# Kernel tuning notes

Hardware: AMD Instinct MI355X
Metric: run time of the kernel (lower is better)

Reference implementation:

```python
import jax, jax.numpy as jnp
import numpy as np

N, S, D, H, E, ETYPES = 1024, 64, 256, 4, 4096, 4
HD = D // H
EPS = 1e-5


def setup_inputs() -> dict:
    key = jax.random.key(0)
    ks = jax.random.split(key, 8)
    node_features = jax.random.normal(ks[0], (N, S, D), dtype=jnp.float32)
    lengths = jax.random.randint(ks[1], (N,), 1, S + 1)
    node_masks = (jnp.arange(S)[None, :] < lengths[:, None]).astype(jnp.float32)
    # unique edges (torch builds an adjacency matrix, so duplicates collapse)
    rng = np.random.default_rng(0)
    cand = rng.integers(0, N, size=(4 * E, 2))
    uniq = np.unique(cand, axis=0)
    assert uniq.shape[0] >= E
    perm = rng.permutation(uniq.shape[0])[:E]
    edge_index = jnp.asarray(uniq[perm].T, dtype=jnp.int64)  # [2, E]
    edge_type = jnp.asarray(rng.integers(1, ETYPES + 1, size=(E,)), dtype=jnp.int64)
    scale = 0.02
    wq = jax.random.normal(ks[2], (D, D), jnp.float32) * scale
    wk = jax.random.normal(ks[3], (D, D), jnp.float32) * scale
    wv = jax.random.normal(ks[4], (D, D), jnp.float32) * scale
    wo = jax.random.normal(ks[5], (D, D), jnp.float32) * scale
    return dict(
        node_features=node_features, node_masks=node_masks,
        ln_w=jnp.ones((D,), jnp.float32), ln_b=jnp.zeros((D,), jnp.float32),
        wq=wq, bq=jnp.zeros((D,), jnp.float32),
        wk=wk, bk=jnp.zeros((D,), jnp.float32),
        wv=wv, bv=jnp.zeros((D,), jnp.float32),
        wo=wo, bo=jnp.zeros((D,), jnp.float32),
        edge_type_weights=jnp.ones((ETYPES,), jnp.float32),
        edge_index=edge_index, edge_type=edge_type,
    )


def reference(node_features, node_masks, ln_w, ln_b, wq, bq, wk, bk, wv, bv,
              wo, bo, edge_type_weights, edge_index, edge_type):
    n, s, d = node_features.shape
    # LayerNorm (biased variance, eps=1e-5, as torch)
    mu = jnp.mean(node_features, axis=-1, keepdims=True)
    var = jnp.mean((node_features - mu) ** 2, axis=-1, keepdims=True)
    xn = (node_features - mu) * jax.lax.rsqrt(var + EPS) * ln_w + ln_b
    q = (xn @ wq + bq).reshape(n, s, H, HD)
    k = (xn @ wk + bk).reshape(n, s, H, HD)
    v = (xn @ wv + bv).reshape(n, s, H, HD)
    src, dst = edge_index[0], edge_index[1]
    # per-edge scalar bias: softplus(edge_type_weights[type-1]).clamp(1e-6, 1e6)
    ew = jnp.clip(jax.nn.softplus(edge_type_weights[edge_type - 1]), 1e-6, 1e6)  # [E]
    qe, ke, ve = q[src], k[dst], v[dst]              # [E,S,H,HD]
    km = node_masks[dst]                              # [E,S] key-side mask
    qm = node_masks[src]                              # [E,S] query-side mask
    scores = jnp.einsum('eqhd,ekhd->ehqk', qe, ke) / jnp.sqrt(jnp.float32(HD))
    scores = scores + ew[:, None, None, None]
    neg = jnp.float32(-1e30)
    scores = jnp.where(km[:, None, None, :] > 0, scores, neg)
    # per-edge softmax over the key node's valid tokens; zero rows where no valid key
    attn = jax.nn.softmax(scores, axis=-1) * km[:, None, None, :]
    ctx = jnp.einsum('ehqk,ekhd->eqhd', attn, ve) * qm[:, :, None, None]  # [E,S,H,HD]
    out = jax.ops.segment_sum(ctx, src, num_segments=n)   # sum over incident edges
    out = out.reshape(n, s, d)
    out = out @ wo + bo                                   # output projection (dropout=eval noop)
    out = out + node_features                             # residual
    return out * node_masks[..., None]
```

## Files before the change

### kernel.cpp

```cpp
#include <hip/hip_runtime.h>

#define DDIM 256
#define NEDGE 4096
#define SLEN 64
#define NNODE 1024
#define ROWS 65536

typedef short s16x8 __attribute__((ext_vector_type(8)));
typedef float f32x4 __attribute__((ext_vector_type(4)));

static __device__ __forceinline__ unsigned short f2bf(float f){
  union { float f; unsigned u; } v; v.f = f;
  unsigned r = v.u + 0x7FFFu + ((v.u >> 16) & 1u);
  return (unsigned short)(r >> 16);
}

static __device__ __forceinline__ void gl2lds16(const unsigned short* g, unsigned short* l){
  __builtin_amdgcn_global_load_lds((const __attribute__((address_space(1))) unsigned int*)g,
                                   (__attribute__((address_space(3))) unsigned int*)l, 16, 0, 0);
}

__global__ __launch_bounds__(256) void setup_kernel(const float* nf, const float* lnw, const float* lnb,
                                                    const float* wq, const float* wk, const float* wv, const float* wo,
                                                    const float* bq, const float* bk, const float* bv,
                                                    const float* masks,
                                                    unsigned short* xn, unsigned short* Wqkv, unsigned short* Wo_t,
                                                    float* qkvb, int* lenp){
  int bid = blockIdx.x, tid = threadIdx.x;
  if (bid < 16384){
    int lane = tid & 63;
    int row = bid*4 + (tid >> 6);
    const float4 x4 = ((const float4*)(nf + (size_t)row*DDIM))[lane];
    float s  = x4.x + x4.y + x4.z + x4.w;
    float sq = x4.x*x4.x + x4.y*x4.y + x4.z*x4.z + x4.w*x4.w;
    for (int off=1; off<64; off<<=1){ s += __shfl_xor(s, off); sq += __shfl_xor(sq, off); }
    float mu  = s  * (1.0f/DDIM);
    float var = sq * (1.0f/DDIM) - mu*mu;
    float rs  = rsqrtf(var + 1e-5f);
    float4 w4 = ((const float4*)lnw)[lane];
    float4 b4 = ((const float4*)lnb)[lane];
    ushort4 o;
    o.x = f2bf((x4.x - mu)*rs*w4.x + b4.x);
    o.y = f2bf((x4.y - mu)*rs*w4.y + b4.y);
    o.z = f2bf((x4.z - mu)*rs*w4.z + b4.z);
    o.w = f2bf((x4.w - mu)*rs*w4.w + b4.w);
    ((ushort4*)(xn + (size_t)row*DDIM))[lane] = o;
  } else if (bid < 17412){
    int idx = (bid - 16384)*256 + tid;
    if (idx < 196608){
      int mat = idx >> 16;
      int rem = idx & 65535;
      int n = rem >> 8, k = rem & 255;
      const float* W = (mat==0)?wq:(mat==1)?wk:wv;
      Wqkv[(size_t)(mat*256 + n)*256 + k] = f2bf(W[k*256 + n]);
    } else if (idx < 262144){
      int rem = idx - 196608;
      int n = rem >> 8, k = rem & 255;
      Wo_t[(size_t)n*256 + k] = f2bf(wo[k*256 + n]);
    } else if (idx < 262912){
      int i = idx - 262144;
      qkvb[i] = (i < 256) ? bq[i] : (i < 512) ? bk[i-256] : bv[i-512];
    }
  } else {
    int lane = tid & 63;
    int node = (bid - 17412)*4 + (tid >> 6);
    unsigned long long b = __ballot(masks[node*SLEN + lane] > 0.f);
    if (lane == 0) lenp[node] = __popcll(b);
  }
}

__global__ void csr_kernel(const int* eidx, int* startp, int* order, int* degp, int* elist){
  __shared__ int deg[NNODE];
  __shared__ int buf[NNODE];
  __shared__ int hist[65];
  __shared__ int cur[NNODE];
  int t = threadIdx.x;
  deg[t] = 0;
  if (t < 65) hist[t] = 0;
  __syncthreads();
  #pragma unroll
  for (int i=0;i<4;i++) atomicAdd(&deg[eidx[i*1024 + t]], 1);
  __syncthreads();
  int d = deg[t];
  buf[t] = d;
  __syncthreads();
  for (int off=1; off<NNODE; off<<=1){
    int v = (t >= off) ? buf[t-off] : 0;
    __syncthreads();
    buf[t] += v;
    __syncthreads();
  }
  int st = buf[t] - d;
  startp[t] = st; degp[t] = d; cur[t] = st;
  int dc = d > 64 ? 64 : d;
  atomicAdd(&hist[dc], 1);
  __syncthreads();
  if (t == 0){
    int acc = 0;
    for (int i=64;i>=0;i--){ int h = hist[i]; hist[i] = acc; acc += h; }
  }
  __syncthreads();
  int pos = atomicAdd(&hist[dc], 1);
  order[pos] = t;
  __syncthreads();
  #pragma unroll
  for (int i=0;i<4;i++){
    int e = i*1024 + t;
    int s = eidx[e];
    int p = atomicAdd(&cur[s], 1);
    elist[p] = eidx[NEDGE + e];
  }
}

__global__ __launch_bounds__(256) void qkv_kernel(const unsigned short* xn, const unsigned short* Wqkv,
                                                  const float* qkvb, const int* lenp,
                                                  unsigned short* qb, unsigned short* kb_, unsigned short* vt){
  __shared__ __align__(16) unsigned short As[4096];
  __shared__ __align__(16) unsigned short Bs[8192];
  int tid = threadIdx.x;
  int lane = tid & 63, wid = tid >> 6, m = lane & 15, quad = lane >> 4;
  int row0 = blockIdx.x * 64;
  int node = row0 >> 6;
  int qtm = (lenp[node] + 15) >> 4;
  int vrows = qtm << 4;
  int col0 = blockIdx.y * 128;
  int rw = (wid & 1) * 32, cw = (wid >> 1) * 64;
  int t0 = rw >> 4;
  f32x4 acc[8];
  #pragma unroll
  for (int i=0;i<8;i++) acc[i] = (f32x4){0.f,0.f,0.f,0.f};
  for (int kc = 0; kc < 4; kc++){
    __syncthreads();
    #pragma unroll
    for (int i=0;i<2;i++){
      if (i*32 + wid*8 < vrows){
        int cid = i*256 + tid, row = cid >> 3, c8 = cid & 7;
        gl2lds16(xn + (size_t)(row0 + row)*DDIM + kc*64 + ((c8 ^ (row&7))<<3), As + cid*8);
      }
    }
    #pragma unroll
    for (int i=0;i<4;i++){
      int cid = i*256 + tid, row = cid >> 3, c8 = cid & 7;
      gl2lds16(Wqkv + (size_t)(col0 + row)*DDIM + kc*64 + ((c8 ^ (row&7))<<3), Bs + cid*8);
    }
    __syncthreads();
    #pragma unroll
    for (int ks=0; ks<2; ks++){
      int sw = ((ks*4 + quad) ^ (m&7)) << 3;
      s16x8 af[2], bf[4];
      #pragma unroll
      for (int mt=0;mt<2;mt++) if (t0 + mt < qtm) af[mt] = *(const s16x8*)(As + (rw + mt*16 + m)*64 + sw);
      #pragma unroll
      for (int nt=0;nt<4;nt++) bf[nt] = *(const s16x8*)(Bs + (cw + nt*16 + m)*64 + sw);
      #pragma unroll
      for (int mt=0;mt<2;mt++) if (t0 + mt < qtm)
        #pragma unroll
        for (int nt=0;nt<4;nt++)
          acc[mt*4+nt] = __builtin_amdgcn_mfma_f32_16x16x32_bf16(af[mt], bf[nt], acc[mt*4+nt], 0,0,0);
    }
  }
  #pragma unroll
  for (int nt=0;nt<4;nt++){
    int cg = col0 + cw + nt*16 + m;
    int mat = cg >> 8, col = cg & 255;
    float bb = qkvb[cg];
    if (mat < 2){
      unsigned short* ob = (mat==0)?qb:kb_;
      #pragma unroll
      for (int mt=0;mt<2;mt++) if (t0 + mt < qtm)
        #pragma unroll
        for (int r=0;r<4;r++){
          int row = row0 + rw + mt*16 + quad*4 + r;
          ob[(size_t)row*DDIM + col] = f2bf(acc[mt*4+nt][r] + bb);
        }
    } else {
      #pragma unroll
      for (int mt=0;mt<2;mt++) if (t0 + mt < qtm){
        int tok0 = rw + mt*16 + quad*4;
        ushort4 p;
        p.x = f2bf(acc[mt*4+nt][0] + bb);
        p.y = f2bf(acc[mt*4+nt][1] + bb);
        p.z = f2bf(acc[mt*4+nt][2] + bb);
        p.w = f2bf(acc[mt*4+nt][3] + bb);
        *(ushort4*)(vt + ((size_t)node*256 + col)*64 + tok0) = p;
      }
    }
  }
}

__global__ __launch_bounds__(256) void attn_kernel(const unsigned short* qb, const unsigned short* kbuf,
                                                   const unsigned short* vtb, const int* lenp,
                                                   const int* startp, const int* degp, const int* elist,
                                                   const int* order, unsigned short* ctxb){
  __shared__ __align__(16) unsigned short Kt[2][4096];
  __shared__ __align__(16) unsigned short Vt[2][4096];
  __shared__ unsigned short P[4096];
  int tid = threadIdx.x;
  int lane = tid & 63, wid = tid >> 6, m = lane & 15, quad = lane >> 4;
  int src = order[blockIdx.x], h = blockIdx.y;
  int ls = lenp[src];
  int qtm = (ls + 15) >> 4;
  int s0 = startp[src], dg = degp[src];
  bool active = wid < qtm;
  unsigned short* Pw = P + wid*1024;

  s16x8 qf0 = {0,0,0,0,0,0,0,0}, qf1 = {0,0,0,0,0,0,0,0};
  if (active){
    const unsigned short* qbase = qb + (size_t)(src*SLEN + wid*16 + m)*DDIM + h*64 + quad*8;
    qf0 = *(const s16x8*)(qbase);
    qf1 = *(const s16x8*)(qbase + 32);
  }
  f32x4 o[4];
  #pragma unroll
  for (int i=0;i<4;i++) o[i] = (f32x4){0.f,0.f,0.f,0.f};

  int dst0 = 0, dst1 = 0, ld0 = 0;
  if (dg > 0){
    dst0 = elist[s0];
    ld0 = lenp[dst0];
    int kch = ((ld0 + 15) >> 4) * 128;
    #pragma unroll
    for (int i=0;i<2;i++){
      int cid = i*256 + tid;
      if (i*256 + wid*64 < kch){
        int row = cid >> 3, c8 = cid & 7;
        gl2lds16(kbuf + (size_t)(dst0*SLEN + row)*DDIM + h*64 + ((c8 ^ (row&7))<<3), Kt[0] + cid*8);
      }
    }
    const unsigned short* vhead = vtb + ((size_t)dst0*256 + h*64)*64;
    #pragma unroll
    for (int i=0;i<2;i++){
      int cid = i*256 + tid, row = cid >> 3, c8 = cid & 7;
      gl2lds16(vhead + row*64 + ((c8 ^ (row&7))<<3), Vt[0] + cid*8);
    }
  }
  if (dg > 1) dst1 = elist[s0 + 1];
  __syncthreads();

  for (int ei=0; ei<dg; ei++){
    int cur = ei & 1, nxt = cur ^ 1;
    int dst2 = (ei+2 < dg) ? elist[s0 + ei + 2] : 0;
    int ld1 = 0;
    if (ei+1 < dg){
      ld1 = lenp[dst1];
      int kch = ((ld1 + 15) >> 4) * 128;
      #pragma unroll
      for (int i=0;i<2;i++){
        int cid = i*256 + tid;
        if (i*256 + wid*64 < kch){
          int row = cid >> 3, c8 = cid & 7;
          gl2lds16(kbuf + (size_t)(dst1*SLEN + row)*DDIM + h*64 + ((c8 ^ (row&7))<<3), Kt[nxt] + cid*8);
        }
      }
      const unsigned short* vhead = vtb + ((size_t)dst1*256 + h*64)*64;
      #pragma unroll
      for (int i=0;i<2;i++){
        int cid = i*256 + tid, row = cid >> 3, c8 = cid & 7;
        gl2lds16(vhead + row*64 + ((c8 ^ (row&7))<<3), Vt[nxt] + cid*8);
      }
    }
    int ktm = (ld0 + 15) >> 4;
    int ks2 = (ktm + 1) >> 1;
    if (active){
      f32x4 acc[4];
      #pragma unroll
      for (int i=0;i<4;i++) acc[i] = (f32x4){0.f,0.f,0.f,0.f};
      #pragma unroll
      for (int kt=0; kt<4; kt++) if (kt < ktm){
        int key = kt*16 + m;
        s16x8 b0 = *(const s16x8*)(Kt[cur] + key*64 + ((quad ^ (m&7))<<3));
        acc[kt] = __builtin_amdgcn_mfma_f32_16x16x32_bf16(qf0, b0, acc[kt], 0,0,0);
        s16x8 b1 = *(const s16x8*)(Kt[cur] + key*64 + (((4 + quad) ^ (m&7))<<3));
        acc[kt] = __builtin_amdgcn_mfma_f32_16x16x32_bf16(qf1, b1, acc[kt], 0,0,0);
      }
      #pragma unroll
      for (int r=0; r<4; r++){
        float x[4];
        #pragma unroll
        for (int kt=0; kt<4; kt++)
          x[kt] = (kt < ktm && kt*16 + m < ld0) ? __expf(acc[kt][r]*0.125f) : 0.f;
        float s = x[0] + x[1] + x[2] + x[3];
        for (int off=1; off<16; off<<=1) s += __shfl_xor(s, off);
        float inv = 1.0f / s;
        int q = quad*4 + r;
        #pragma unroll
        for (int kt=0; kt<4; kt++) if (kt < 2*ks2){
          int key = kt*16 + m;
          Pw[q*64 + (((key>>3)^(q&7))<<3) + (key&7)] = f2bf(x[kt]*inv);
        }
      }
      #pragma unroll
      for (int ks=0; ks<2; ks++) if (ks < ks2){
        s16x8 pa = *(const s16x8*)(Pw + m*64 + ((((ks*4+quad))^(m&7))<<3));
        #pragma unroll
        for (int dt=0; dt<4; dt++){
          int d = dt*16 + m;
          s16x8 vf = *(const s16x8*)(Vt[cur] + d*64 + (((ks*4+quad)^(d&7))<<3));
          o[dt] = __builtin_amdgcn_mfma_f32_16x16x32_bf16(pa, vf, o[dt], 0,0,0);
        }
      }
    }
    dst0 = dst1; ld0 = ld1; dst1 = dst2;
    __syncthreads();
  }
  if (active){
    #pragma unroll
    for (int dt=0; dt<4; dt++){
      int col = h*64 + dt*16 + m;
      #pragma unroll
      for (int r=0; r<4; r++){
        int row = src*SLEN + wid*16 + quad*4 + r;
        ctxb[(size_t)row*DDIM + col] = f2bf(o[dt][r]);
      }
    }
  }
}

__global__ __launch_bounds__(256) void out_kernel(const unsigned short* ctxb, const unsigned short* Wo_t,
                                                  const float* bo, const float* nf, const float* masks,
                                                  const int* lenp, float* out){
  __shared__ __align__(16) unsigned short As[4096];
  __shared__ __align__(16) unsigned short Bs[8192];
  int tid = threadIdx.x;
  int lane = tid & 63, wid = tid >> 6, m = lane & 15, quad = lane >> 4;
  int row0 = blockIdx.x * 64;
  int node = row0 >> 6;
  int qtm = (lenp[node] + 15) >> 4;
  int vrows = qtm << 4;
  int col0 = blockIdx.y * 128;
  int rw = (wid & 1) * 32, cw = (wid >> 1) * 64;
  int t0 = rw >> 4;
  f32x4 acc[8];
  #pragma unroll
  for (int i=0;i<8;i++) acc[i] = (f32x4){0.f,0.f,0.f,0.f};
  for (int kc = 0; kc < 4; kc++){
    __syncthreads();
    #pragma unroll
    for (int i=0;i<2;i++){
      if (i*32 + wid*8 < vrows){
        int cid = i*256 + tid, row = cid >> 3, c8 = cid & 7;
        gl2lds16(ctxb + (size_t)(row0 + row)*DDIM + kc*64 + ((c8 ^ (row&7))<<3), As + cid*8);
      }
    }
    #pragma unroll
    for (int i=0;i<4;i++){
      int cid = i*256 + tid, row = cid >> 3, c8 = cid & 7;
      gl2lds16(Wo_t + (size_t)(col0 + row)*DDIM + kc*64 + ((c8 ^ (row&7))<<3), Bs + cid*8);
    }
    __syncthreads();
    #pragma unroll
    for (int ks=0; ks<2; ks++){
      int sw = ((ks*4 + quad) ^ (m&7)) << 3;
      s16x8 af[2], bf[4];
      #pragma unroll
      for (int mt=0;mt<2;mt++) if (t0 + mt < qtm) af[mt] = *(const s16x8*)(As + (rw + mt*16 + m)*64 + sw);
      #pragma unroll
      for (int nt=0;nt<4;nt++) bf[nt] = *(const s16x8*)(Bs + (cw + nt*16 + m)*64 + sw);
      #pragma unroll
      for (int mt=0;mt<2;mt++) if (t0 + mt < qtm)
        #pragma unroll
        for (int nt=0;nt<4;nt++)
          acc[mt*4+nt] = __builtin_amdgcn_mfma_f32_16x16x32_bf16(af[mt], bf[nt], acc[mt*4+nt], 0,0,0);
    }
  }
  #pragma unroll
  for (int nt=0;nt<4;nt++){
    int col = col0 + cw + nt*16 + m;
    float bb = bo[col];
    #pragma unroll
    for (int mt=0;mt<2;mt++){
      if (t0 + mt < qtm){
        #pragma unroll
        for (int r=0;r<4;r++){
          int row = row0 + rw + mt*16 + quad*4 + r;
          float v = acc[mt*4+nt][r] + bb + nf[(size_t)row*DDIM + col];
          out[(size_t)row*DDIM + col] = v * masks[row];
        }
      } else {
        #pragma unroll
        for (int r=0;r<4;r++){
          int row = row0 + rw + mt*16 + quad*4 + r;
          out[(size_t)row*DDIM + col] = 0.f;
        }
      }
    }
  }
}

extern "C" void kernel_launch(void* const* d_in, const int* in_sizes, int n_in,
                              void* d_out, int out_size, void* d_ws, size_t ws_size,
                              hipStream_t stream){
  const float* nf    = (const float*)d_in[0];
  const float* masks = (const float*)d_in[1];
  const float* lnw   = (const float*)d_in[2];
  const float* lnb   = (const float*)d_in[3];
  const float* wq    = (const float*)d_in[4];
  const float* bq    = (const float*)d_in[5];
  const float* wk    = (const float*)d_in[6];
  const float* bk    = (const float*)d_in[7];
  const float* wv    = (const float*)d_in[8];
  const float* bv    = (const float*)d_in[9];
  const float* wo    = (const float*)d_in[10];
  const float* bo    = (const float*)d_in[11];
  const int*   eidx  = (const int*)d_in[13];
  float* out = (float*)d_out;

  char* ws = (char*)d_ws;
  const size_t B = (size_t)ROWS * DDIM * 2;
  unsigned short* xn   = (unsigned short*)(ws);
  unsigned short* qb   = (unsigned short*)(ws + B);
  unsigned short* kb   = (unsigned short*)(ws + 2*B);
  unsigned short* vt   = (unsigned short*)(ws + 3*B);
  unsigned short* ctxb = (unsigned short*)(ws + 4*B);
  char* wp = ws + 5*B;
  unsigned short* Wqkv = (unsigned short*)(wp);
  unsigned short* Wo_t = (unsigned short*)(wp + 393216);
  float* qkvb         = (float*)(wp + 524288);
  char* ip = wp + 528384;
  int* startp = (int*)(ip);
  int* lenp   = (int*)(ip + 4096);
  int* order  = (int*)(ip + 8192);
  int* degp   = (int*)(ip + 12288);
  int* elist  = (int*)(ip + 16384);

  setup_kernel<<<17668, 256, 0, stream>>>(nf, lnw, lnb, wq, wk, wv, wo, bq, bk, bv,
                                          masks, xn, Wqkv, Wo_t, qkvb, lenp);
  csr_kernel<<<1, 1024, 0, stream>>>(eidx, startp, order, degp, elist);
  qkv_kernel<<<dim3(ROWS/64, 6), 256, 0, stream>>>(xn, Wqkv, qkvb, lenp, qb, kb, vt);
  attn_kernel<<<dim3(NNODE, 4), 256, 0, stream>>>(qb, kb, vt, lenp, startp, degp, elist, order, ctxb);
  out_kernel<<<dim3(ROWS/64, 2), 256, 0, stream>>>(ctxb, Wo_t, bo, nf, masks, lenp, out);
}
```

Before: 345.7 us.

## Restructure QKV and output GEMMs to direct-load per-node tiles; skip padded LN rows

The QKV and output projection kernels no longer stage tiles in LDS. Each block now covers one node's full 64 rows, and each wave loads its bf16 fragments straight from global memory for 64 columns. Q is stored transposed (feature-major) like V, so the attention kernel gathers Q fragments with strided scalar loads. LayerNorm also returns early for rows past the node's 16-padded valid length, and the output kernel zero-fills padded rows with vector stores. This removes LDS traffic, barriers and redundant A-tile loads, at the cost of uncoalesced global fragment loads and a strided scalar Q gather.

```diff
diff --git a/kernel.cpp b/kernel.cpp
--- a/kernel.cpp
+++ b/kernel.cpp
@@ -30,6 +30,11 @@
   if (bid < 16384){
     int lane = tid & 63;
     int row = bid*4 + (tid >> 6);
+    int node = row >> 6;
+    unsigned long long bm = __ballot(masks[node*SLEN + lane] > 0.f);
+    int len = __popcll(bm);
+    int vrows = ((len + 15) >> 4) << 4;
+    if ((row & 63) >= vrows) return;
     const float4 x4 = ((const float4*)(nf + (size_t)row*DDIM))[lane];
     float s  = x4.x + x4.y + x4.z + x4.w;
     float sq = x4.x*x4.x + x4.y*x4.y + x4.z*x4.z + x4.w*x4.w;
@@ -114,81 +119,65 @@
 
 __global__ __launch_bounds__(256) void qkv_kernel(const unsigned short* xn, const unsigned short* Wqkv,
                                                   const float* qkvb, const int* lenp,
-                                                  unsigned short* qb, unsigned short* kb_, unsigned short* vt){
-  __shared__ __align__(16) unsigned short As[4096];
-  __shared__ __align__(16) unsigned short Bs[8192];
+                                                  unsigned short* qt, unsigned short* kb_, unsigned short* vt){
   int tid = threadIdx.x;
   int lane = tid & 63, wid = tid >> 6, m = lane & 15, quad = lane >> 4;
-  int row0 = blockIdx.x * 64;
-  int node = row0 >> 6;
+  int node = blockIdx.x;
+  int row0 = node * 64;
   int qtm = (lenp[node] + 15) >> 4;
-  int vrows = qtm << 4;
-  int col0 = blockIdx.y * 128;
-  int rw = (wid & 1) * 32, cw = (wid >> 1) * 64;
-  int t0 = rw >> 4;
-  f32x4 acc[8];
-  #pragma unroll
-  for (int i=0;i<8;i++) acc[i] = (f32x4){0.f,0.f,0.f,0.f};
-  for (int kc = 0; kc < 4; kc++){
-    __syncthreads();
-    #pragma unroll
-    for (int i=0;i<2;i++){
-      if (i*32 + wid*8 < vrows){
-        int cid = i*256 + tid, row = cid >> 3, c8 = cid & 7;
-        gl2lds16(xn + (size_t)(row0 + row)*DDIM + kc*64 + ((c8 ^ (row&7))<<3), As + cid*8);
-      }
-    }
-    #pragma unroll
-    for (int i=0;i<4;i++){
-      int cid = i*256 + tid, row = cid >> 3, c8 = cid & 7;
-      gl2lds16(Wqkv + (size_t)(col0 + row)*DDIM + kc*64 + ((c8 ^ (row&7))<<3), Bs + cid*8);
-    }
-    __syncthreads();
-    #pragma unroll
-    for (int ks=0; ks<2; ks++){
-      int sw = ((ks*4 + quad) ^ (m&7)) << 3;
-      s16x8 af[2], bf[4];
-      #pragma unroll
-      for (int mt=0;mt<2;mt++) if (t0 + mt < qtm) af[mt] = *(const s16x8*)(As + (rw + mt*16 + m)*64 + sw);
-      #pragma unroll
-      for (int nt=0;nt<4;nt++) bf[nt] = *(const s16x8*)(Bs + (cw + nt*16 + m)*64 + sw);
-      #pragma unroll
-      for (int mt=0;mt<2;mt++) if (t0 + mt < qtm)
-        #pragma unroll
-        for (int nt=0;nt<4;nt++)
-          acc[mt*4+nt] = __builtin_amdgcn_mfma_f32_16x16x32_bf16(af[mt], bf[nt], acc[mt*4+nt], 0,0,0);
-    }
-  }
-  #pragma unroll
-  for (int nt=0;nt<4;nt++){
-    int cg = col0 + cw + nt*16 + m;
-    int mat = cg >> 8, col = cg & 255;
-    float bb = qkvb[cg];
-    if (mat < 2){
-      unsigned short* ob = (mat==0)?qb:kb_;
-      #pragma unroll
-      for (int mt=0;mt<2;mt++) if (t0 + mt < qtm)
+  int by = blockIdx.y;
+  int cb = wid * 64;
+  f32x4 acc[16];
+  #pragma unroll
+  for (int i=0;i<16;i++) acc[i] = (f32x4){0.f,0.f,0.f,0.f};
+  const unsigned short* ab = xn   + (size_t)(row0 + m)*DDIM + quad*8;
+  const unsigned short* bb = Wqkv + ((size_t)by*256 + cb + m)*DDIM + quad*8;
+  #pragma unroll
+  for (int ks=0; ks<8; ks++){
+    s16x8 bf[4];
+    #pragma unroll
+    for (int nt=0;nt<4;nt++) bf[nt] = *(const s16x8*)(bb + nt*16*DDIM + ks*32);
+    #pragma unroll
+    for (int mt=0;mt<4;mt++) if (mt < qtm){
+      s16x8 af = *(const s16x8*)(ab + mt*16*DDIM + ks*32);
+      #pragma unroll
+      for (int nt=0;nt<4;nt++)
+        acc[mt*4+nt] = __builtin_amdgcn_mfma_f32_16x16x32_bf16(af, bf[nt], acc[mt*4+nt], 0,0,0);
+    }
+  }
+  if (by != 1){
+    unsigned short* dst = (by==0) ? qt : vt;
+    #pragma unroll
+    for (int nt=0;nt<4;nt++){
+      int col = cb + nt*16 + m;
+      float bbv = qkvb[by*256 + col];
+      #pragma unroll
+      for (int mt=0;mt<4;mt++) if (mt < qtm){
+        ushort4 p;
+        p.x = f2bf(acc[mt*4+nt][0] + bbv);
+        p.y = f2bf(acc[mt*4+nt][1] + bbv);
+        p.z = f2bf(acc[mt*4+nt][2] + bbv);
+        p.w = f2bf(acc[mt*4+nt][3] + bbv);
+        *(ushort4*)(dst + ((size_t)node*256 + col)*64 + mt*16 + quad*4) = p;
+      }
+    }
+  } else {
+    #pragma unroll
+    for (int nt=0;nt<4;nt++){
+      int col = cb + nt*16 + m;
+      float bbv = qkvb[256 + col];
+      #pragma unroll
+      for (int mt=0;mt<4;mt++) if (mt < qtm)
         #pragma unroll
         for (int r=0;r<4;r++){
-          int row = row0 + rw + mt*16 + quad*4 + r;
-          ob[(size_t)row*DDIM + col] = f2bf(acc[mt*4+nt][r] + bb);
+          int row = row0 + mt*16 + quad*4 + r;
+          kb_[(size_t)row*DDIM + col] = f2bf(acc[mt*4+nt][r] + bbv);
         }
-    } else {
-      #pragma unroll
-      for (int mt=0;mt<2;mt++) if (t0 + mt < qtm){
-        int tok0 = rw + mt*16 + quad*4;
-        ushort4 p;
-        p.x = f2bf(acc[mt*4+nt][0] + bb);
-        p.y = f2bf(acc[mt*4+nt][1] + bb);
-        p.z = f2bf(acc[mt*4+nt][2] + bb);
-        p.w = f2bf(acc[mt*4+nt][3] + bb);
-        *(ushort4*)(vt + ((size_t)node*256 + col)*64 + tok0) = p;
-      }
-    }
-  }
-}
-
-__global__ __launch_bounds__(256) void attn_kernel(const unsigned short* qb, const unsigned short* kbuf,
+    }
+  }
+}
+
+__global__ __launch_bounds__(256) void attn_kernel(const unsigned short* qt, const unsigned short* kbuf,
                                                    const unsigned short* vtb, const int* lenp,
                                                    const int* startp, const int* degp, const int* elist,
                                                    const int* order, unsigned short* ctxb){
@@ -206,9 +195,13 @@
 
   s16x8 qf0 = {0,0,0,0,0,0,0,0}, qf1 = {0,0,0,0,0,0,0,0};
   if (active){
-    const unsigned short* qbase = qb + (size_t)(src*SLEN + wid*16 + m)*DDIM + h*64 + quad*8;
-    qf0 = *(const s16x8*)(qbase);
-    qf1 = *(const s16x8*)(qbase + 32);
+    const unsigned short* qtb = qt + ((size_t)src*256 + h*64)*64;
+    int tok = wid*16 + m;
+    #pragma unroll
+    for (int j=0;j<8;j++){
+      qf0[j] = (short)qtb[(quad*8 + j)*64 + tok];
+      qf1[j] = (short)qtb[(32 + quad*8 + j)*64 + tok];
+    }
   }
   f32x4 o[4];
   #pragma unroll
@@ -319,72 +312,46 @@
 __global__ __launch_bounds__(256) void out_kernel(const unsigned short* ctxb, const unsigned short* Wo_t,
                                                   const float* bo, const float* nf, const float* masks,
                                                   const int* lenp, float* out){
-  __shared__ __align__(16) unsigned short As[4096];
-  __shared__ __align__(16) unsigned short Bs[8192];
   int tid = threadIdx.x;
   int lane = tid & 63, wid = tid >> 6, m = lane & 15, quad = lane >> 4;
-  int row0 = blockIdx.x * 64;
-  int node = row0 >> 6;
+  int node = blockIdx.x;
+  int row0 = node * 64;
   int qtm = (lenp[node] + 15) >> 4;
   int vrows = qtm << 4;
-  int col0 = blockIdx.y * 128;
-  int rw = (wid & 1) * 32, cw = (wid >> 1) * 64;
-  int t0 = rw >> 4;
-  f32x4 acc[8];
-  #pragma unroll
-  for (int i=0;i<8;i++) acc[i] = (f32x4){0.f,0.f,0.f,0.f};
-  for (int kc = 0; kc < 4; kc++){
-    __syncthreads();
-    #pragma unroll
-    for (int i=0;i<2;i++){
-      if (i*32 + wid*8 < vrows){
-        int cid = i*256 + tid, row = cid >> 3, c8 = cid & 7;
-        gl2lds16(ctxb + (size_t)(row0 + row)*DDIM + kc*64 + ((c8 ^ (row&7))<<3), As + cid*8);
-      }
-    }
-    #pragma unroll
-    for (int i=0;i<4;i++){
-      int cid = i*256 + tid, row = cid >> 3, c8 = cid & 7;
-      gl2lds16(Wo_t + (size_t)(col0 + row)*DDIM + kc*64 + ((c8 ^ (row&7))<<3), Bs + cid*8);
-    }
-    __syncthreads();
-    #pragma unroll
-    for (int ks=0; ks<2; ks++){
-      int sw = ((ks*4 + quad) ^ (m&7)) << 3;
-      s16x8 af[2], bf[4];
-      #pragma unroll
-      for (int mt=0;mt<2;mt++) if (t0 + mt < qtm) af[mt] = *(const s16x8*)(As + (rw + mt*16 + m)*64 + sw);
-      #pragma unroll
-      for (int nt=0;nt<4;nt++) bf[nt] = *(const s16x8*)(Bs + (cw + nt*16 + m)*64 + sw);
-      #pragma unroll
-      for (int mt=0;mt<2;mt++) if (t0 + mt < qtm)
-        #pragma unroll
-        for (int nt=0;nt<4;nt++)
-          acc[mt*4+nt] = __builtin_amdgcn_mfma_f32_16x16x32_bf16(af[mt], bf[nt], acc[mt*4+nt], 0,0,0);
+  int cb = wid * 64;
+  f32x4 acc[16];
+  #pragma unroll
+  for (int i=0;i<16;i++) acc[i] = (f32x4){0.f,0.f,0.f,0.f};
+  const unsigned short* ab = ctxb + (size_t)(row0 + m)*DDIM + quad*8;
+  const unsigned short* bb = Wo_t + (size_t)(cb + m)*DDIM + quad*8;
+  #pragma unroll
+  for (int ks=0; ks<8; ks++){
+    s16x8 bf[4];
+    #pragma unroll
+    for (int nt=0;nt<4;nt++) bf[nt] = *(const s16x8*)(bb + nt*16*DDIM + ks*32);
+    #pragma unroll
+    for (int mt=0;mt<4;mt++) if (mt < qtm){
+      s16x8 af = *(const s16x8*)(ab + mt*16*DDIM + ks*32);
+      #pragma unroll
+      for (int nt=0;nt<4;nt++)
+        acc[mt*4+nt] = __builtin_amdgcn_mfma_f32_16x16x32_bf16(af, bf[nt], acc[mt*4+nt], 0,0,0);
     }
   }
   #pragma unroll
   for (int nt=0;nt<4;nt++){
-    int col = col0 + cw + nt*16 + m;
-    float bb = bo[col];
-    #pragma unroll
-    for (int mt=0;mt<2;mt++){
-      if (t0 + mt < qtm){
-        #pragma unroll
-        for (int r=0;r<4;r++){
-          int row = row0 + rw + mt*16 + quad*4 + r;
-          float v = acc[mt*4+nt][r] + bb + nf[(size_t)row*DDIM + col];
-          out[(size_t)row*DDIM + col] = v * masks[row];
-        }
-      } else {
-        #pragma unroll
-        for (int r=0;r<4;r++){
-          int row = row0 + rw + mt*16 + quad*4 + r;
-          out[(size_t)row*DDIM + col] = 0.f;
-        }
-      }
-    }
-  }
+    int col = cb + nt*16 + m;
+    float bbv = bo[col];
+    #pragma unroll
+    for (int mt=0;mt<4;mt++) if (mt < qtm)
+      #pragma unroll
+      for (int r=0;r<4;r++){
+        int row = row0 + mt*16 + quad*4 + r;
+        float v = acc[mt*4+nt][r] + bbv + nf[(size_t)row*DDIM + col];
+        out[(size_t)row*DDIM + col] = v * masks[row];
+      }
+  }
+  for (int r = vrows + wid; r < 64; r += 4)
+    ((float4*)(out + (size_t)(row0 + r)*DDIM))[lane] = (float4){0.f,0.f,0.f,0.f};
 }
 
 extern "C" void kernel_launch(void* const* d_in, const int* in_sizes, int n_in,
@@ -408,7 +375,7 @@
   char* ws = (char*)d_ws;
   const size_t B = (size_t)ROWS * DDIM * 2;
   unsigned short* xn   = (unsigned short*)(ws);
-  unsigned short* qb   = (unsigned short*)(ws + B);
+  unsigned short* qt   = (unsigned short*)(ws + B);
   unsigned short* kb   = (unsigned short*)(ws + 2*B);
   unsigned short* vt   = (unsigned short*)(ws + 3*B);
   unsigned short* ctxb = (unsigned short*)(ws + 4*B);
@@ -426,7 +393,7 @@
   setup_kernel<<<17668, 256, 0, stream>>>(nf, lnw, lnb, wq, wk, wv, wo, bq, bk, bv,
                                           masks, xn, Wqkv, Wo_t, qkvb, lenp);
   csr_kernel<<<1, 1024, 0, stream>>>(eidx, startp, order, degp, elist);
-  qkv_kernel<<<dim3(ROWS/64, 6), 256, 0, stream>>>(xn, Wqkv, qkvb, lenp, qb, kb, vt);
-  attn_kernel<<<dim3(NNODE, 4), 256, 0, stream>>>(qb, kb, vt, lenp, startp, degp, elist, order, ctxb);
-  out_kernel<<<dim3(ROWS/64, 2), 256, 0, stream>>>(ctxb, Wo_t, bo, nf, masks, lenp, out);
-}
+  qkv_kernel<<<dim3(NNODE, 3), 256, 0, stream>>>(xn, Wqkv, qkvb, lenp, qt, kb, vt);
+  attn_kernel<<<dim3(NNODE, 4), 256, 0, stream>>>(qt, kb, vt, lenp, startp, degp, elist, order, ctxb);
+  out_kernel<<<NNODE, 256, 0, stream>>>(ctxb, Wo_t, bo, nf, masks, lenp, out);
+}
```

Result: slower. 384.4 us (+11.2%).

## Merge CSR build into setup, skip padded LayerNorm rows, one block per node in attention

Applied to the files above, without the earlier changes.

The CSR build moves into an extra block of the setup kernel, removing one launch and its single-block serial tail. The LayerNorm path now skips rows beyond each node's padded valid length, since those rows are never read. Attention now runs one block per source node, with each wave handling one head across all query tiles. Each neighbour's full K/V tile is loaded once for all four heads instead of once per head, but the double-buffered prefetch is dropped and register pressure rises with 16 accumulators per wave.

```diff
diff --git a/kernel.cpp b/kernel.cpp
--- a/kernel.cpp
+++ b/kernel.cpp
@@ -23,13 +23,23 @@
 __global__ __launch_bounds__(256) void setup_kernel(const float* nf, const float* lnw, const float* lnb,
                                                     const float* wq, const float* wk, const float* wv, const float* wo,
                                                     const float* bq, const float* bk, const float* bv,
-                                                    const float* masks,
+                                                    const float* masks, const int* eidx,
                                                     unsigned short* xn, unsigned short* Wqkv, unsigned short* Wo_t,
-                                                    float* qkvb, int* lenp){
+                                                    float* qkvb, int* lenp,
+                                                    int* startp, int* order, int* degp, int* elist){
+  __shared__ int sdeg[NNODE];
+  __shared__ int sbuf[256];
+  __shared__ int scur[NNODE];
+  __shared__ int shist[65];
   int bid = blockIdx.x, tid = threadIdx.x;
   if (bid < 16384){
     int lane = tid & 63;
     int row = bid*4 + (tid >> 6);
+    int node = row >> 6;
+    unsigned long long bm = __ballot(masks[node*SLEN + lane] > 0.f);
+    int len = __popcll(bm);
+    int vrows = ((len + 15) >> 4) << 4;
+    if ((row & 63) >= vrows) return;
     const float4 x4 = ((const float4*)(nf + (size_t)row*DDIM))[lane];
     float s  = x4.x + x4.y + x4.z + x4.w;
     float sq = x4.x*x4.x + x4.y*x4.y + x4.z*x4.z + x4.w*x4.w;
@@ -61,54 +71,63 @@
       int i = idx - 262144;
       qkvb[i] = (i < 256) ? bq[i] : (i < 512) ? bk[i-256] : bv[i-512];
     }
-  } else {
+  } else if (bid < 17668){
     int lane = tid & 63;
     int node = (bid - 17412)*4 + (tid >> 6);
     unsigned long long b = __ballot(masks[node*SLEN + lane] > 0.f);
     if (lane == 0) lenp[node] = __popcll(b);
-  }
-}
-
-__global__ void csr_kernel(const int* eidx, int* startp, int* order, int* degp, int* elist){
-  __shared__ int deg[NNODE];
-  __shared__ int buf[NNODE];
-  __shared__ int hist[65];
-  __shared__ int cur[NNODE];
-  int t = threadIdx.x;
-  deg[t] = 0;
-  if (t < 65) hist[t] = 0;
-  __syncthreads();
-  #pragma unroll
-  for (int i=0;i<4;i++) atomicAdd(&deg[eidx[i*1024 + t]], 1);
-  __syncthreads();
-  int d = deg[t];
-  buf[t] = d;
-  __syncthreads();
-  for (int off=1; off<NNODE; off<<=1){
-    int v = (t >= off) ? buf[t-off] : 0;
-    __syncthreads();
-    buf[t] += v;
-    __syncthreads();
-  }
-  int st = buf[t] - d;
-  startp[t] = st; degp[t] = d; cur[t] = st;
-  int dc = d > 64 ? 64 : d;
-  atomicAdd(&hist[dc], 1);
-  __syncthreads();
-  if (t == 0){
-    int acc = 0;
-    for (int i=64;i>=0;i--){ int h = hist[i]; hist[i] = acc; acc += h; }
-  }
-  __syncthreads();
-  int pos = atomicAdd(&hist[dc], 1);
-  order[pos] = t;
-  __syncthreads();
-  #pragma unroll
-  for (int i=0;i<4;i++){
-    int e = i*1024 + t;
-    int s = eidx[e];
-    int p = atomicAdd(&cur[s], 1);
-    elist[p] = eidx[NEDGE + e];
+  } else {
+    int t = tid;
+    #pragma unroll
+    for (int i=0;i<4;i++) sdeg[i*256 + t] = 0;
+    if (t < 65) shist[t] = 0;
+    __syncthreads();
+    #pragma unroll
+    for (int i=0;i<16;i++) atomicAdd(&sdeg[eidx[i*256 + t]], 1);
+    __syncthreads();
+    int d[4];
+    #pragma unroll
+    for (int j=0;j<4;j++) d[j] = sdeg[t*4 + j];
+    int s = d[0] + d[1] + d[2] + d[3];
+    sbuf[t] = s;
+    __syncthreads();
+    for (int off=1; off<256; off<<=1){
+      int v = (t >= off) ? sbuf[t-off] : 0;
+      __syncthreads();
+      sbuf[t] += v;
+      __syncthreads();
+    }
+    int base = sbuf[t] - s;
+    int acc = base;
+    #pragma unroll
+    for (int j=0;j<4;j++){
+      int node = t*4 + j;
+      startp[node] = acc; degp[node] = d[j]; scur[node] = acc;
+      acc += d[j];
+      int dc = d[j] > 64 ? 64 : d[j];
+      atomicAdd(&shist[dc], 1);
+    }
+    __syncthreads();
+    if (t == 0){
+      int a = 0;
+      for (int i=64;i>=0;i--){ int h = shist[i]; shist[i] = a; a += h; }
+    }
+    __syncthreads();
+    #pragma unroll
+    for (int j=0;j<4;j++){
+      int node = t*4 + j;
+      int dc = d[j] > 64 ? 64 : d[j];
+      int pos = atomicAdd(&shist[dc], 1);
+      order[pos] = node;
+    }
+    __syncthreads();
+    #pragma unroll
+    for (int i=0;i<16;i++){
+      int e = i*256 + t;
+      int sn = eidx[e];
+      int p = atomicAdd(&scur[sn], 1);
+      elist[p] = eidx[NEDGE + e];
+    }
   }
 }
 
@@ -192,93 +211,73 @@
                                                    const unsigned short* vtb, const int* lenp,
                                                    const int* startp, const int* degp, const int* elist,
                                                    const int* order, unsigned short* ctxb){
-  __shared__ __align__(16) unsigned short Kt[2][4096];
-  __shared__ __align__(16) unsigned short Vt[2][4096];
+  __shared__ __align__(16) unsigned short Kf[16384];
+  __shared__ __align__(16) unsigned short Vf[16384];
   __shared__ unsigned short P[4096];
   int tid = threadIdx.x;
-  int lane = tid & 63, wid = tid >> 6, m = lane & 15, quad = lane >> 4;
-  int src = order[blockIdx.x], h = blockIdx.y;
+  int lane = tid & 63, h = tid >> 6, m = lane & 15, quad = lane >> 4;
+  int src = order[blockIdx.x];
   int ls = lenp[src];
   int qtm = (ls + 15) >> 4;
   int s0 = startp[src], dg = degp[src];
-  bool active = wid < qtm;
-  unsigned short* Pw = P + wid*1024;
-
-  s16x8 qf0 = {0,0,0,0,0,0,0,0}, qf1 = {0,0,0,0,0,0,0,0};
-  if (active){
-    const unsigned short* qbase = qb + (size_t)(src*SLEN + wid*16 + m)*DDIM + h*64 + quad*8;
-    qf0 = *(const s16x8*)(qbase);
-    qf1 = *(const s16x8*)(qbase + 32);
-  }
-  f32x4 o[4];
-  #pragma unroll
-  for (int i=0;i<4;i++) o[i] = (f32x4){0.f,0.f,0.f,0.f};
-
-  int dst0 = 0, dst1 = 0, ld0 = 0;
-  if (dg > 0){
-    dst0 = elist[s0];
-    ld0 = lenp[dst0];
-    int kch = ((ld0 + 15) >> 4) * 128;
-    #pragma unroll
-    for (int i=0;i<2;i++){
+  unsigned short* Pw = P + h*1024;
+
+  s16x8 qf[4][2];
+  #pragma unroll
+  for (int qt_=0; qt_<4; qt_++) if (qt_ < qtm){
+    const unsigned short* qbase = qb + (size_t)(src*SLEN + qt_*16 + m)*DDIM + h*64 + quad*8;
+    qf[qt_][0] = *(const s16x8*)(qbase);
+    qf[qt_][1] = *(const s16x8*)(qbase + 32);
+  }
+  f32x4 o[16];
+  #pragma unroll
+  for (int i=0;i<16;i++) o[i] = (f32x4){0.f,0.f,0.f,0.f};
+
+  int dst = 0, ld = 0;
+  if (dg > 0){ dst = elist[s0]; ld = lenp[dst]; }
+
+  for (int ei=0; ei<dg; ei++){
+    int dstn = (ei+1 < dg) ? elist[s0 + ei + 1] : 0;
+    int ktm = (ld + 15) >> 4;
+    int ks2 = (ktm + 1) >> 1;
+    int krows = ktm << 4;
+    __syncthreads();
+    #pragma unroll
+    for (int i=0;i<8;i++){
       int cid = i*256 + tid;
-      if (i*256 + wid*64 < kch){
-        int row = cid >> 3, c8 = cid & 7;
-        gl2lds16(kbuf + (size_t)(dst0*SLEN + row)*DDIM + h*64 + ((c8 ^ (row&7))<<3), Kt[0] + cid*8);
-      }
-    }
-    const unsigned short* vhead = vtb + ((size_t)dst0*256 + h*64)*64;
-    #pragma unroll
-    for (int i=0;i<2;i++){
-      int cid = i*256 + tid, row = cid >> 3, c8 = cid & 7;
-      gl2lds16(vhead + row*64 + ((c8 ^ (row&7))<<3), Vt[0] + cid*8);
-    }
-  }
-  if (dg > 1) dst1 = elist[s0 + 1];
-  __syncthreads();
-
-  for (int ei=0; ei<dg; ei++){
-    int cur = ei & 1, nxt = cur ^ 1;
-    int dst2 = (ei+2 < dg) ? elist[s0 + ei + 2] : 0;
-    int ld1 = 0;
-    if (ei+1 < dg){
-      ld1 = lenp[dst1];
-      int kch = ((ld1 + 15) >> 4) * 128;
-      #pragma unroll
-      for (int i=0;i<2;i++){
-        int cid = i*256 + tid;
-        if (i*256 + wid*64 < kch){
-          int row = cid >> 3, c8 = cid & 7;
-          gl2lds16(kbuf + (size_t)(dst1*SLEN + row)*DDIM + h*64 + ((c8 ^ (row&7))<<3), Kt[nxt] + cid*8);
-        }
-      }
-      const unsigned short* vhead = vtb + ((size_t)dst1*256 + h*64)*64;
-      #pragma unroll
-      for (int i=0;i<2;i++){
-        int cid = i*256 + tid, row = cid >> 3, c8 = cid & 7;
-        gl2lds16(vhead + row*64 + ((c8 ^ (row&7))<<3), Vt[nxt] + cid*8);
-      }
-    }
-    int ktm = (ld0 + 15) >> 4;
-    int ks2 = (ktm + 1) >> 1;
-    if (active){
+      int tok = cid >> 5;
+      if (tok < krows){
+        int within = cid & 31, seg = within >> 3, c8 = within & 7;
+        gl2lds16(kbuf + (size_t)(dst*SLEN + tok)*DDIM + seg*64 + ((c8 ^ (tok&7))<<3), Kf + cid*8);
+      }
+    }
+    #pragma unroll
+    for (int i=0;i<8;i++){
+      int cid = i*256 + tid;
+      int col = cid >> 3, t8 = cid & 7;
+      gl2lds16(vtb + ((size_t)dst*256 + col)*64 + ((t8 ^ (col&7))<<3), Vf + cid*8);
+    }
+    int ldn = (ei+1 < dg) ? lenp[dstn] : 0;
+    __syncthreads();
+    #pragma unroll
+    for (int qt_=0; qt_<4; qt_++) if (qt_ < qtm){
       f32x4 acc[4];
       #pragma unroll
       for (int i=0;i<4;i++) acc[i] = (f32x4){0.f,0.f,0.f,0.f};
       #pragma unroll
       for (int kt=0; kt<4; kt++) if (kt < ktm){
         int key = kt*16 + m;
-        s16x8 b0 = *(const s16x8*)(Kt[cur] + key*64 + ((quad ^ (m&7))<<3));
-        acc[kt] = __builtin_amdgcn_mfma_f32_16x16x32_bf16(qf0, b0, acc[kt], 0,0,0);
-        s16x8 b1 = *(const s16x8*)(Kt[cur] + key*64 + (((4 + quad) ^ (m&7))<<3));
-        acc[kt] = __builtin_amdgcn_mfma_f32_16x16x32_bf16(qf1, b1, acc[kt], 0,0,0);
+        s16x8 b0 = *(const s16x8*)(Kf + key*DDIM + h*64 + ((quad ^ (key&7))<<3));
+        acc[kt] = __builtin_amdgcn_mfma_f32_16x16x32_bf16(qf[qt_][0], b0, acc[kt], 0,0,0);
+        s16x8 b1 = *(const s16x8*)(Kf + key*DDIM + h*64 + (((4 + quad) ^ (key&7))<<3));
+        acc[kt] = __builtin_amdgcn_mfma_f32_16x16x32_bf16(qf[qt_][1], b1, acc[kt], 0,0,0);
       }
       #pragma unroll
       for (int r=0; r<4; r++){
         float x[4];
         #pragma unroll
         for (int kt=0; kt<4; kt++)
-          x[kt] = (kt < ktm && kt*16 + m < ld0) ? __expf(acc[kt][r]*0.125f) : 0.f;
+          x[kt] = (kt < ktm && kt*16 + m < ld) ? __expf(acc[kt][r]*0.125f) : 0.f;
         float s = x[0] + x[1] + x[2] + x[3];
         for (int off=1; off<16; off<<=1) s += __shfl_xor(s, off);
         float inv = 1.0f / s;
@@ -286,7 +285,7 @@
         #pragma unroll
         for (int kt=0; kt<4; kt++) if (kt < 2*ks2){
           int key = kt*16 + m;
-          Pw[q*64 + (((key>>3)^(q&7))<<3) + (key&7)] = f2bf(x[kt]*inv);
+          Pw[q*64 + (((key>>3)^(q&7))<<3) + (key&7)] = f2bf((kt < ktm) ? x[kt]*inv : 0.f);
         }
       }
       #pragma unroll
@@ -294,23 +293,23 @@
         s16x8 pa = *(const s16x8*)(Pw + m*64 + ((((ks*4+quad))^(m&7))<<3));
         #pragma unroll
         for (int dt=0; dt<4; dt++){
-          int d = dt*16 + m;
-          s16x8 vf = *(const s16x8*)(Vt[cur] + d*64 + (((ks*4+quad)^(d&7))<<3));
-          o[dt] = __builtin_amdgcn_mfma_f32_16x16x32_bf16(pa, vf, o[dt], 0,0,0);
+          int col = h*64 + dt*16 + m;
+          s16x8 vf = *(const s16x8*)(Vf + col*64 + (((ks*4+quad)^(col&7))<<3));
+          o[qt_*4+dt] = __builtin_amdgcn_mfma_f32_16x16x32_bf16(pa, vf, o[qt_*4+dt], 0,0,0);
         }
       }
     }
-    dst0 = dst1; ld0 = ld1; dst1 = dst2;
-    __syncthreads();
-  }
-  if (active){
+    dst = dstn; ld = ldn;
+  }
+  #pragma unroll
+  for (int qt_=0; qt_<4; qt_++) if (qt_ < qtm){
     #pragma unroll
     for (int dt=0; dt<4; dt++){
       int col = h*64 + dt*16 + m;
       #pragma unroll
       for (int r=0; r<4; r++){
-        int row = src*SLEN + wid*16 + quad*4 + r;
-        ctxb[(size_t)row*DDIM + col] = f2bf(o[dt][r]);
+        int row = src*SLEN + qt_*16 + quad*4 + r;
+        ctxb[(size_t)row*DDIM + col] = f2bf(o[qt_*4+dt][r]);
       }
     }
   }
@@ -423,10 +422,10 @@
   int* degp   = (int*)(ip + 12288);
   int* elist  = (int*)(ip + 16384);
 
-  setup_kernel<<<17668, 256, 0, stream>>>(nf, lnw, lnb, wq, wk, wv, wo, bq, bk, bv,
-                                          masks, xn, Wqkv, Wo_t, qkvb, lenp);
-  csr_kernel<<<1, 1024, 0, stream>>>(eidx, startp, order, degp, elist);
-  qkv_kernel<<<dim3(ROWS/64, 6), 256, 0, stream>>>(xn, Wqkv, qkvb, lenp, qb, kb, vt);
-  attn_kernel<<<dim3(NNODE, 4), 256, 0, stream>>>(qb, kb, vt, lenp, startp, degp, elist, order, ctxb);
-  out_kernel<<<dim3(ROWS/64, 2), 256, 0, stream>>>(ctxb, Wo_t, bo, nf, masks, lenp, out);
-}
+  setup_kernel<<<17669, 256, 0, stream>>>(nf, lnw, lnb, wq, wk, wv, wo, bq, bk, bv,
+                                          masks, eidx, xn, Wqkv, Wo_t, qkvb, lenp,
+                                          startp, order, degp, elist);
+  qkv_kernel<<<dim3(NNODE, 6), 256, 0, stream>>>(xn, Wqkv, qkvb, lenp, qb, kb, vt);
+  attn_kernel<<<NNODE, 256, 0, stream>>>(qb, kb, vt, lenp, startp, degp, elist, order, ctxb);
+  out_kernel<<<dim3(NNODE, 2), 256, 0, stream>>>(ctxb, Wo_t, bo, nf, masks, lenp, out);
+}
```

After: 361.5 us. +4.5%, slower.
